# Kernel optimization log

Hardware: AMD Instinct MI355X
Metric: run time of the kernel (lower is better)

## Reference

```python
import jax, jax.numpy as jnp
import numpy as np

B, T, E, H, LBL = 32, 2048, 256, 256, 20


def _lstm_cell_step(x, W_ih, b_ih, b_hh):
    # Single LSTM cell step from zero state (h0=c0=0): W_hh @ h0 == 0.
    # x: [B, T, E]; W_ih: [4H, E]; gate order in torch: i, f, g, o
    gates = jnp.einsum('bte,ge->btg', x, W_ih) + b_ih + b_hh  # [B, T, 4H]
    i, f, g, o = jnp.split(gates, 4, axis=-1)
    c = jax.nn.sigmoid(i) * jnp.tanh(g)  # f * c0 == 0
    return jax.nn.sigmoid(o) * jnp.tanh(c)  # [B, T, H]


def setup_inputs() -> dict:
    key = jax.random.key(0)
    ks = jax.random.split(key, 12)
    s_ih = 1.0 / np.sqrt(H)
    inp = {
        'X': jax.random.normal(ks[0], (B, T, E), dtype=jnp.float32),
        'lengths': jax.random.randint(ks[1], (B,), 1, T + 1, dtype=jnp.int32),
        'W_ih_f': jax.random.uniform(ks[2], (4 * H, E), jnp.float32, -s_ih, s_ih),
        'b_ih_f': jax.random.uniform(ks[3], (4 * H,), jnp.float32, -s_ih, s_ih),
        'b_hh_f': jax.random.uniform(ks[4], (4 * H,), jnp.float32, -s_ih, s_ih),
        'W_ih_r': jax.random.uniform(ks[5], (4 * H, E), jnp.float32, -s_ih, s_ih),
        'b_ih_r': jax.random.uniform(ks[6], (4 * H,), jnp.float32, -s_ih, s_ih),
        'b_hh_r': jax.random.uniform(ks[7], (4 * H,), jnp.float32, -s_ih, s_ih),
        'W1': jax.random.uniform(ks[8], (256, 4 * H), jnp.float32, -1 / np.sqrt(4 * H), 1 / np.sqrt(4 * H)),
        'b1': jax.random.uniform(ks[9], (256,), jnp.float32, -1 / np.sqrt(4 * H), 1 / np.sqrt(4 * H)),
        'W2': jax.random.uniform(ks[10], (LBL, 256), jnp.float32, -1 / 16.0, 1 / 16.0),
        'b2': jax.random.uniform(ks[11], (LBL,), jnp.float32, -1 / 16.0, 1 / 16.0),
    }
    return inp


def reference(X, lengths, W_ih_f, b_ih_f, b_hh_f, W_ih_r, b_ih_r, b_hh_r, W1, b1, W2, b2):
    lengths = jnp.clip(lengths, 1, T).astype(jnp.int32)
    # Both directions are independent single-step cells (seq_len==1 in original)
    h_f = _lstm_cell_step(X, W_ih_f, b_ih_f, b_hh_f)  # [B, T, H]
    h_r = _lstm_cell_step(X, W_ih_r, b_ih_r, b_hh_r)  # [B, T, H]
    s = jnp.concatenate([h_f, h_r], axis=-1)          # [B, T, 2H]
    mask = (jnp.arange(T)[None, :] < lengths[:, None])  # [B, T]
    m = mask[:, :, None].astype(s.dtype)
    avg_pool = (s * m).sum(axis=1) / lengths[:, None].astype(s.dtype)  # [B, 2H]
    NEG = jnp.asarray(-1e30, s.dtype)
    max_pool = jnp.where(mask[:, :, None], s, NEG).max(axis=1)          # [B, 2H]
    doc = jnp.concatenate([avg_pool, max_pool], axis=-1)                # [B, 4H]
    rel = jax.nn.relu(doc)
    d1 = rel @ W1.T + b1        # dropout is identity in eval mode
    return d1 @ W2.T + b2        # [B, LBL]
```

## Files before the change

### kernel.cpp

```cpp
#include <hip/hip_runtime.h>
#include <stdint.h>

#define B_   32
#define T_   2048
#define E_   256
#define H_   256
#define LBL_ 20
#define M_   (B_ * T_)
#define NPACK_ 1536

typedef __attribute__((ext_vector_type(8))) short bf16x8;
typedef __attribute__((ext_vector_type(4))) float f32x4;

__device__ __forceinline__ unsigned short f2bf(float f) {
    union { float f; unsigned int u; } a; a.f = f;
    unsigned int u = a.u;
    u += 0x7FFFu + ((u >> 16) & 1u);
    return (unsigned short)(u >> 16);
}

__device__ __forceinline__ float rcp_(float x) {
#if __has_builtin(__builtin_amdgcn_rcpf)
    return __builtin_amdgcn_rcpf(x);
#else
    return 1.0f / x;
#endif
}
__device__ __forceinline__ float exp2_(float x) {
#if __has_builtin(__builtin_amdgcn_exp2f)
    return __builtin_amdgcn_exp2f(x);
#else
    return exp2f(x);
#endif
}
__device__ __forceinline__ float sigm_(float x) {
    return rcp_(1.f + exp2_(x * -1.44269504f));
}
__device__ __forceinline__ float tanhs_(float x) {
    return __builtin_fmaf(-2.f, rcp_(1.f + exp2_(x * 2.88539008f)), 1.f);
}
__device__ __forceinline__ float tanhp_(float c) {
    float t = c * c;
    float num = c * __builtin_fmaf(t, t + 105.f, 945.f);
    float den = __builtin_fmaf(t, __builtin_fmaf(t, 15.f, 420.f), 945.f);
    return num * rcp_(den);
}

__global__ __launch_bounds__(256) void prep(
    const float4* __restrict__ X4, uint4* __restrict__ Xb4,
    const int* __restrict__ lengths,
    const float* __restrict__ Wf, const float* __restrict__ bif, const float* __restrict__ bhf,
    const float* __restrict__ Wr, const float* __restrict__ bir, const float* __restrict__ bhr,
    unsigned short* __restrict__ Wp, float* __restrict__ bias_p)
{
    int bi = blockIdx.x;
    if (bi < 8192) {
        int b = bi >> 8, tile = bi & 255;
        int lenb = lengths[b]; lenb = lenb < 1 ? 1 : (lenb > T_ ? T_ : lenb);
        int used = (lenb + 127) & ~127;
        if (tile * 8 >= used) return;
        int idx = b * 65536 + tile * 256 + threadIdx.x;
        float4 v0 = X4[2 * idx], v1 = X4[2 * idx + 1];
        union { unsigned short us[8]; uint4 u; } r;
        r.us[0] = f2bf(v0.x); r.us[1] = f2bf(v0.y); r.us[2] = f2bf(v0.z); r.us[3] = f2bf(v0.w);
        r.us[4] = f2bf(v1.x); r.us[5] = f2bf(v1.y); r.us[6] = f2bf(v1.z); r.us[7] = f2bf(v1.w);
        Xb4[idx] = r.u;
    } else {
        int n = bi - 8192, t = threadIdx.x;
        int gidx = n / 48, r = n % 48;
        int ty = r >> 4, cc = r & 15;
        int dir = gidx >> 4, c = (gidx & 15) * 16 + cc;
        int gate = (ty == 0) ? 0 : (ty == 1 ? 2 : 3);
        int wrow = gate * 256 + c;
        const float* W = dir ? Wr : Wf;
        Wp[n * 256 + t] = f2bf(W[wrow * 256 + t]);
        if (t == 0)
            bias_p[n] = (dir ? bir[wrow] : bif[wrow]) + (dir ? bhr[wrow] : bhf[wrow]);
    }
}

__global__ __launch_bounds__(256, 2) void gemm_pool(
    const unsigned short* __restrict__ Xb, const unsigned short* __restrict__ Wp,
    const float* __restrict__ bias_p, const int* __restrict__ lengths,
    float* __restrict__ psum, float* __restrict__ pmax)
{
    __shared__ __align__(16) short tiles[2][1792 * 8];
    __shared__ float red[2][4][2][16];

    const int tid  = threadIdx.x;
    const int w    = tid >> 6;
    const int lane = tid & 63;
    const int g    = blockIdx.x;
    const int m_tile = ((g >> 7) << 3) + (g & 7);
    const int n_tile = (g >> 3) & 15;
    const int m0   = m_tile << 7;
    const int n0   = n_tile * 96;

    const int b  = m0 >> 11;
    const int t0 = m0 & 2047;
    int lenb = lengths[b]; lenb = lenb < 1 ? 1 : (lenb > T_ ? T_ : lenb);

    if (t0 >= lenb) {
        if (tid < 32) {
            int gg = tid >> 4, c16 = tid & 15;
            int gidx = n_tile * 2 + gg;
            int col2 = (gidx >> 4) * 256 + (gidx & 15) * 16 + c16;
            int mt = m_tile & 15;
            psum[(b * 16 + mt) * 512 + col2] = 0.f;
            pmax[(b * 16 + mt) * 512 + col2] = -1e30f;
        }
        return;
    }

    const unsigned short* gp[7];
    int lbs[7];
    #pragma unroll
    for (int r = 0; r < 7; ++r) {
        int base_slot = r * 256 + w * 64;
        int s = base_slot + lane;
        int isA = (s < 1024);
        int sl = isA ? s : (s - 1024);
        int row = sl >> 3;
        int kb = (s & 7) ^ (row & 7);
        gp[r] = isA ? (Xb + (m0 + row) * 256 + kb * 8)
                    : (Wp + (n0 + row) * 256 + kb * 8);
        lbs[r] = base_slot * 8;
    }

    f32x4 acc[2][6];
    #pragma unroll
    for (int i = 0; i < 2; ++i)
        #pragma unroll
        for (int j = 0; j < 6; ++j) acc[i][j] = (f32x4){0.f, 0.f, 0.f, 0.f};

    #pragma unroll
    for (int r = 0; r < 7; ++r)
        __builtin_amdgcn_global_load_lds(
            (const __attribute__((address_space(1))) void*)(gp[r]),
            (__attribute__((address_space(3))) void*)(&tiles[0][0] + lbs[r]),
            16, 0, 0);

    #pragma unroll
    for (int kit = 0; kit < 4; ++kit) {
        __syncthreads();
        if (kit < 3) {
            #pragma unroll
            for (int r = 0; r < 7; ++r)
                __builtin_amdgcn_global_load_lds(
                    (const __attribute__((address_space(1))) void*)(gp[r] + (kit + 1) * 64),
                    (__attribute__((address_space(3))) void*)(&tiles[(kit + 1) & 1][0] + lbs[r]),
                    16, 0, 0);
        }
        const short* As = &tiles[kit & 1][0];
        const short* Bs = As + 1024 * 8;

        #pragma unroll
        for (int ks = 0; ks < 2; ++ks) {
            bf16x8 af[2], bfr[6];
            int kb = ks * 4 + (lane >> 4);
            #pragma unroll
            for (int rt = 0; rt < 2; ++rt) {
                int row = w * 32 + rt * 16 + (lane & 15);
                af[rt] = *(const bf16x8*)(As + (row * 8 + (kb ^ (row & 7))) * 8);
            }
            #pragma unroll
            for (int ct = 0; ct < 6; ++ct) {
                int row = ct * 16 + (lane & 15);
                bfr[ct] = *(const bf16x8*)(Bs + (row * 8 + (kb ^ (row & 7))) * 8);
            }
            #pragma unroll
            for (int rt = 0; rt < 2; ++rt)
                #pragma unroll
                for (int ct = 0; ct < 6; ++ct)
                    acc[rt][ct] = __builtin_amdgcn_mfma_f32_16x16x32_bf16(
                        af[rt], bfr[ct], acc[rt][ct], 0, 0, 0);
        }
    }

    const int q = lane >> 4, cc = lane & 15;

    #pragma unroll
    for (int gg = 0; gg < 2; ++gg) {
        float bi = bias_p[n0 + gg * 48 + 0  + cc];
        float bg = bias_p[n0 + gg * 48 + 16 + cc];
        float bo = bias_p[n0 + gg * 48 + 32 + cc];
        float hsum = 0.f, hmax = -1e30f;
        #pragma unroll
        for (int rt = 0; rt < 2; ++rt) {
            if (t0 + w * 32 + rt * 16 >= lenb) continue;
            #pragma unroll
            for (int reg = 0; reg < 4; ++reg) {
                int row = w * 32 + rt * 16 + q * 4 + reg;
                int t = t0 + row;
                float iv = acc[rt][gg * 3 + 0][reg] + bi;
                float gv = acc[rt][gg * 3 + 1][reg] + bg;
                float ov = acc[rt][gg * 3 + 2][reg] + bo;
                float cv = sigm_(iv) * tanhs_(gv);
                float h  = sigm_(ov) * tanhp_(cv);
                if (t < lenb) { hsum += h; hmax = fmaxf(hmax, h); }
            }
        }
        hsum += __shfl_xor(hsum, 16, 64);
        hmax = fmaxf(hmax, __shfl_xor(hmax, 16, 64));
        hsum += __shfl_xor(hsum, 32, 64);
        hmax = fmaxf(hmax, __shfl_xor(hmax, 32, 64));
        if (q == 0) { red[0][w][gg][cc] = hsum; red[1][w][gg][cc] = hmax; }
    }
    __syncthreads();
    if (tid < 32) {
        int gg = tid >> 4, c16 = tid & 15;
        float s  = red[0][0][gg][c16] + red[0][1][gg][c16] + red[0][2][gg][c16] + red[0][3][gg][c16];
        float mx = fmaxf(fmaxf(red[1][0][gg][c16], red[1][1][gg][c16]),
                         fmaxf(red[1][2][gg][c16], red[1][3][gg][c16]));
        int gidx = n_tile * 2 + gg;
        int col2 = (gidx >> 4) * 256 + (gidx & 15) * 16 + c16;
        int mt = m_tile & 15;
        psum[(b * 16 + mt) * 512 + col2] = s;
        pmax[(b * 16 + mt) * 512 + col2] = mx;
    }
}

__global__ __launch_bounds__(256) void mlp1(
    const float* __restrict__ psum, const float* __restrict__ pmax,
    const int* __restrict__ lengths,
    const float* __restrict__ W1, const float* __restrict__ b1,
    float* __restrict__ d1g)
{
    __shared__ float doc[1024];
    int nt = blockIdx.x, b = blockIdx.y, tid = threadIdx.x;
    int lenb = lengths[b]; lenb = lenb < 1 ? 1 : (lenb > T_ ? T_ : lenb);
    float invlen = 1.f / (float)lenb;
    for (int col = tid; col < 512; col += 256) {
        float s = 0.f, mx = -1e30f;
        #pragma unroll
        for (int mt = 0; mt < 16; ++mt) {
            s += psum[(b * 16 + mt) * 512 + col];
            mx = fmaxf(mx, pmax[(b * 16 + mt) * 512 + col]);
        }
        doc[col]       = fmaxf(s * invlen, 0.f);
        doc[512 + col] = fmaxf(mx, 0.f);
    }
    __syncthreads();
    int neuron = tid >> 2, tq = tid & 3;
    int row = nt * 64 + neuron;
    const float4* wrow = (const float4*)(W1 + row * 1024 + tq * 256);
    const float4* dv   = (const float4*)doc + tq * 64;
    float a0 = 0.f, a1 = 0.f, a2 = 0.f, a3 = 0.f;
    #pragma unroll 4
    for (int k = 0; k < 64; ++k) {
        float4 wv = wrow[k]; float4 xv = dv[k];
        a0 += wv.x * xv.x; a1 += wv.y * xv.y; a2 += wv.z * xv.z; a3 += wv.w * xv.w;
    }
    float a = a0 + a1 + a2 + a3;
    a += __shfl_xor(a, 1, 64);
    a += __shfl_xor(a, 2, 64);
    if (tq == 0) d1g[b * 256 + row] = a + b1[row];
}

__global__ __launch_bounds__(256) void mlp2(
    const float* __restrict__ d1g,
    const float* __restrict__ W2, const float* __restrict__ b2,
    float* __restrict__ out)
{
    __shared__ float d1s[256];
    int b = blockIdx.x, tid = threadIdx.x;
    d1s[tid] = d1g[b * 256 + tid];
    __syncthreads();
    int j = tid >> 3, tq = tid & 7;
    float a = 0.f;
    if (j < LBL_) {
        const float4* wr = (const float4*)(W2 + j * 256) + tq * 8;
        const float4* dd = (const float4*)d1s + tq * 8;
        #pragma unroll
        for (int k = 0; k < 8; ++k) {
            float4 wv = wr[k]; float4 xv = dd[k];
            a += wv.x * xv.x + wv.y * xv.y + wv.z * xv.z + wv.w * xv.w;
        }
    }
    a += __shfl_xor(a, 1, 64);
    a += __shfl_xor(a, 2, 64);
    a += __shfl_xor(a, 4, 64);
    if (j < LBL_ && tq == 0) out[b * LBL_ + j] = a + b2[j];
}

#define XB_OFF   0u
#define WP_OFF   33554432u
#define BIAS_OFF 34340864u
#define PSUM_OFF 34347008u
#define PMAX_OFF 35395584u
#define D1_OFF   36444160u

extern "C" void kernel_launch(void* const* d_in, const int* in_sizes, int n_in,
                              void* d_out, int out_size, void* d_ws, size_t ws_size,
                              hipStream_t stream) {
    (void)in_sizes; (void)n_in; (void)out_size; (void)ws_size;
    const float* X      = (const float*)d_in[0];
    const int*   lens   = (const int*)d_in[1];
    const float* W_ih_f = (const float*)d_in[2];
    const float* b_ih_f = (const float*)d_in[3];
    const float* b_hh_f = (const float*)d_in[4];
    const float* W_ih_r = (const float*)d_in[5];
    const float* b_ih_r = (const float*)d_in[6];
    const float* b_hh_r = (const float*)d_in[7];
    const float* W1     = (const float*)d_in[8];
    const float* b1     = (const float*)d_in[9];
    const float* W2     = (const float*)d_in[10];
    const float* b2     = (const float*)d_in[11];
    float* out = (float*)d_out;

    char* ws = (char*)d_ws;
    unsigned short* Xb     = (unsigned short*)(ws + XB_OFF);
    unsigned short* Wp     = (unsigned short*)(ws + WP_OFF);
    float*          bias_p = (float*)(ws + BIAS_OFF);
    float*          psum   = (float*)(ws + PSUM_OFF);
    float*          pmax   = (float*)(ws + PMAX_OFF);
    float*          d1g    = (float*)(ws + D1_OFF);

    prep<<<dim3(8192 + NPACK_), 256, 0, stream>>>(
        (const float4*)X, (uint4*)Xb, lens,
        W_ih_f, b_ih_f, b_hh_f, W_ih_r, b_ih_r, b_hh_r, Wp, bias_p);
    gemm_pool<<<dim3(8192), 256, 0, stream>>>(Xb, Wp, bias_p, lens, psum, pmax);
    mlp1<<<dim3(4, 32), 256, 0, stream>>>(psum, pmax, lens, W1, b1, d1g);
    mlp2<<<dim3(B_), 256, 0, stream>>>(d1g, W2, b2, out);
}
```

Measured before the change: 198.6 us.

## Keep full W tile in LDS, stream A fragments to registers, fuse activation reciprocals

The GEMM kernel now loads the whole 96x256 weight tile into LDS once. A-operand fragments are read straight from global memory into double-buffered registers, which removes the per-K-step LDS staging and barriers. The sigmoid/tanh math is merged so fewer reciprocals are needed per element. Skipped tiles no longer write zero partials; instead mlp1 reduces only over the valid m-tiles. Occupancy is raised to 3 blocks per SM, at the cost of uncoalesced-ish direct global A loads and a larger register footprint.

```diff
diff --git a/kernel.cpp b/kernel.cpp
--- a/kernel.cpp
+++ b/kernel.cpp
@@ -32,18 +32,6 @@
 #else
     return exp2f(x);
 #endif
-}
-__device__ __forceinline__ float sigm_(float x) {
-    return rcp_(1.f + exp2_(x * -1.44269504f));
-}
-__device__ __forceinline__ float tanhs_(float x) {
-    return __builtin_fmaf(-2.f, rcp_(1.f + exp2_(x * 2.88539008f)), 1.f);
-}
-__device__ __forceinline__ float tanhp_(float c) {
-    float t = c * c;
-    float num = c * __builtin_fmaf(t, t + 105.f, 945.f);
-    float den = __builtin_fmaf(t, __builtin_fmaf(t, 15.f, 420.f), 945.f);
-    return num * rcp_(den);
 }
 
 __global__ __launch_bounds__(256) void prep(
@@ -79,12 +67,12 @@
     }
 }
 
-__global__ __launch_bounds__(256, 2) void gemm_pool(
+__global__ __launch_bounds__(256, 3) void gemm_pool(
     const unsigned short* __restrict__ Xb, const unsigned short* __restrict__ Wp,
     const float* __restrict__ bias_p, const int* __restrict__ lengths,
     float* __restrict__ psum, float* __restrict__ pmax)
 {
-    __shared__ __align__(16) short tiles[2][1792 * 8];
+    __shared__ __align__(16) short Bs[96 * 256];
     __shared__ float red[2][4][2][16];
 
     const int tid  = threadIdx.x;
@@ -100,31 +88,17 @@
     const int t0 = m0 & 2047;
     int lenb = lengths[b]; lenb = lenb < 1 ? 1 : (lenb > T_ ? T_ : lenb);
 
-    if (t0 >= lenb) {
-        if (tid < 32) {
-            int gg = tid >> 4, c16 = tid & 15;
-            int gidx = n_tile * 2 + gg;
-            int col2 = (gidx >> 4) * 256 + (gidx & 15) * 16 + c16;
-            int mt = m_tile & 15;
-            psum[(b * 16 + mt) * 512 + col2] = 0.f;
-            pmax[(b * 16 + mt) * 512 + col2] = -1e30f;
-        }
-        return;
-    }
-
-    const unsigned short* gp[7];
-    int lbs[7];
-    #pragma unroll
-    for (int r = 0; r < 7; ++r) {
-        int base_slot = r * 256 + w * 64;
-        int s = base_slot + lane;
-        int isA = (s < 1024);
-        int sl = isA ? s : (s - 1024);
-        int row = sl >> 3;
-        int kb = (s & 7) ^ (row & 7);
-        gp[r] = isA ? (Xb + (m0 + row) * 256 + kb * 8)
-                    : (Wp + (n0 + row) * 256 + kb * 8);
-        lbs[r] = base_slot * 8;
+    if (t0 >= lenb) return;
+
+    #pragma unroll
+    for (int rr = 0; rr < 12; ++rr) {
+        int s = rr * 256 + tid;
+        int row = s >> 5, kcs = s & 31;
+        int kc = (kcs & 24) | ((kcs & 7) ^ (row & 7));
+        __builtin_amdgcn_global_load_lds(
+            (const __attribute__((address_space(1))) void*)(Wp + (n0 + row) * 256 + kc * 8),
+            (__attribute__((address_space(3))) void*)(Bs + (rr * 256 + (w << 6)) * 8),
+            16, 0, 0);
     }
 
     f32x4 acc[2][6];
@@ -133,51 +107,52 @@
         #pragma unroll
         for (int j = 0; j < 6; ++j) acc[i][j] = (f32x4){0.f, 0.f, 0.f, 0.f};
 
-    #pragma unroll
-    for (int r = 0; r < 7; ++r)
-        __builtin_amdgcn_global_load_lds(
-            (const __attribute__((address_space(1))) void*)(gp[r]),
-            (__attribute__((address_space(3))) void*)(&tiles[0][0] + lbs[r]),
-            16, 0, 0);
+    const int rowa = m0 + w * 32 + (lane & 15);
+    const int q    = lane >> 4;
+    const unsigned short* Abase = Xb + rowa * 256 + q * 8;
+
+    bf16x8 aU[4], aV[4];
+    #pragma unroll
+    for (int ks = 0; ks < 2; ++ks)
+        #pragma unroll
+        for (int rt = 0; rt < 2; ++rt)
+            aU[ks * 2 + rt] = *(const bf16x8*)(Abase + rt * 16 * 256 + ks * 4 * 8);
+
+    __syncthreads();
 
     #pragma unroll
     for (int kit = 0; kit < 4; ++kit) {
-        __syncthreads();
+        bf16x8* cur = (kit & 1) ? aV : aU;
+        bf16x8* nxt = (kit & 1) ? aU : aV;
         if (kit < 3) {
             #pragma unroll
-            for (int r = 0; r < 7; ++r)
-                __builtin_amdgcn_global_load_lds(
-                    (const __attribute__((address_space(1))) void*)(gp[r] + (kit + 1) * 64),
-                    (__attribute__((address_space(3))) void*)(&tiles[(kit + 1) & 1][0] + lbs[r]),
-                    16, 0, 0);
-        }
-        const short* As = &tiles[kit & 1][0];
-        const short* Bs = As + 1024 * 8;
-
+            for (int ks = 0; ks < 2; ++ks)
+                #pragma unroll
+                for (int rt = 0; rt < 2; ++rt)
+                    nxt[ks * 2 + rt] = *(const bf16x8*)(Abase + rt * 16 * 256
+                                                        + ((kit + 1) * 8 + ks * 4) * 8);
+        }
         #pragma unroll
         for (int ks = 0; ks < 2; ++ks) {
-            bf16x8 af[2], bfr[6];
-            int kb = ks * 4 + (lane >> 4);
-            #pragma unroll
-            for (int rt = 0; rt < 2; ++rt) {
-                int row = w * 32 + rt * 16 + (lane & 15);
-                af[rt] = *(const bf16x8*)(As + (row * 8 + (kb ^ (row & 7))) * 8);
-            }
+            bf16x8 bfr[6];
+            int kc = kit * 8 + ks * 4 + q;
             #pragma unroll
             for (int ct = 0; ct < 6; ++ct) {
-                int row = ct * 16 + (lane & 15);
-                bfr[ct] = *(const bf16x8*)(Bs + (row * 8 + (kb ^ (row & 7))) * 8);
+                int rb = ct * 16 + (lane & 15);
+                int slot = rb * 32 + (kc & 24) + ((kc & 7) ^ (rb & 7));
+                bfr[ct] = *(const bf16x8*)(Bs + slot * 8);
             }
             #pragma unroll
             for (int rt = 0; rt < 2; ++rt)
                 #pragma unroll
                 for (int ct = 0; ct < 6; ++ct)
                     acc[rt][ct] = __builtin_amdgcn_mfma_f32_16x16x32_bf16(
-                        af[rt], bfr[ct], acc[rt][ct], 0, 0, 0);
-        }
-    }
-
-    const int q = lane >> 4, cc = lane & 15;
+                        cur[ks * 2 + rt], bfr[ct], acc[rt][ct], 0, 0, 0);
+        }
+    }
+
+    const int cc = lane & 15;
+    const float L2E = 1.44269504f;
 
     #pragma unroll
     for (int gg = 0; gg < 2; ++gg) {
@@ -195,8 +170,14 @@
                 float iv = acc[rt][gg * 3 + 0][reg] + bi;
                 float gv = acc[rt][gg * 3 + 1][reg] + bg;
                 float ov = acc[rt][gg * 3 + 2][reg] + bo;
-                float cv = sigm_(iv) * tanhs_(gv);
-                float h  = sigm_(ov) * tanhp_(cv);
+                float e1 = exp2_(iv * -L2E);
+                float e2 = exp2_(gv * -2.f * L2E);
+                float e3 = exp2_(ov * -L2E);
+                float cv = (1.f - e2) * rcp_((1.f + e1) * (1.f + e2));
+                float tt  = cv * cv;
+                float num = cv * __builtin_fmaf(tt, tt + 105.f, 945.f);
+                float den = __builtin_fmaf(tt, __builtin_fmaf(tt, 15.f, 420.f), 945.f);
+                float h = num * rcp_(den * (1.f + e3));
                 if (t < lenb) { hsum += h; hmax = fmaxf(hmax, h); }
             }
         }
@@ -229,11 +210,11 @@
     __shared__ float doc[1024];
     int nt = blockIdx.x, b = blockIdx.y, tid = threadIdx.x;
     int lenb = lengths[b]; lenb = lenb < 1 ? 1 : (lenb > T_ ? T_ : lenb);
+    int cnt = (lenb + 127) >> 7;
     float invlen = 1.f / (float)lenb;
     for (int col = tid; col < 512; col += 256) {
         float s = 0.f, mx = -1e30f;
-        #pragma unroll
-        for (int mt = 0; mt < 16; ++mt) {
+        for (int mt = 0; mt < cnt; ++mt) {
             s += psum[(b * 16 + mt) * 512 + col];
             mx = fmaxf(mx, pmax[(b * 16 + mt) * 512 + col]);
         }
```

After: 204.2 us. +2.8%, slower.
